# Kernel optimization log

Hardware: AMD Instinct MI355X
Metric: run time of the kernel (lower is better)

## Reference

```python
import jax, jax.numpy as jnp
import numpy as np

B, D, H, W = 16, 128, 128, 128
MAX_K = 3  # max(possible_k=(1,3))
ROT_AXES = (1, 2)  # spatial_axes=(0,1) -> dims (1,2) of [B,D,H,W]


def setup_inputs() -> dict:
    key = jax.random.key(0)
    k1, k2, k3, k4 = jax.random.split(key, 4)
    volume = jax.random.normal(k1, (B, D, H, W), dtype=jnp.float32)
    gt_mask = jax.random.uniform(k2, (B, D, H, W), dtype=jnp.float32)
    gt_skel = jax.random.uniform(k3, (B, D, H, W), dtype=jnp.float32)
    # per-sample rotation count koefs = apply_transform * possible_k[idx]; values in [0, MAX_K]
    koefs = jax.random.randint(k4, (B,), 0, MAX_K + 1, dtype=jnp.int32)
    return {"volume": volume, "gt_mask": gt_mask, "gt_skel": gt_skel, "koefs": koefs}


def reference(volume, gt_mask, gt_skel, koefs):
    # Iterative per-sample masked rot90, exactly as the torch loop:
    # each step rotates the full batch once more and blends where koefs >= step.
    for rotate_num in range(1, MAX_K + 1):
        apply = (koefs >= rotate_num)[:, None, None, None]
        volume = jnp.where(apply, jnp.rot90(volume, k=1, axes=ROT_AXES), volume)
        gt_mask = jnp.where(apply, jnp.rot90(gt_mask, k=1, axes=ROT_AXES), gt_mask)
        gt_skel = jnp.where(apply, jnp.rot90(gt_skel, k=1, axes=ROT_AXES), gt_skel)
    return (volume, gt_mask, gt_skel)
```

## Files before the change

### kernel.cpp

```cpp
#include <hip/hip_runtime.h>


typedef float f32x4 __attribute__((ext_vector_type(4)));

#define NN 128
#define W4 32
#define SAMPLE (NN * NN * W4)
#define PER_TENSOR (16 * SAMPLE)
#define TPB 256
#define BLOCKS 2048

__global__ __launch_bounds__(TPB) void rot90_gather_kernel(
    const f32x4* __restrict__ vol,
    const f32x4* __restrict__ msk,
    const f32x4* __restrict__ skl,
    const int* __restrict__ koefs,
    f32x4* __restrict__ out)
{
    const int tid = blockIdx.x * TPB + threadIdx.x;
    const int i  = (tid >> 12) & 127;
    const int j  = (tid >> 5) & 127;
    const int w4 = tid & 31;

    const int s0 = (i * NN + j) * W4 + w4;
    const int s1 = (j * NN + (127 - i)) * W4 + w4;
    const int s2 = ((127 - i) * NN + (127 - j)) * W4 + w4;
    const int s3 = ((127 - j) * NN + i) * W4 + w4;

    int off[16];
#pragma unroll
    for (int b = 0; b < 16; ++b) {
        const int k = koefs[b];
        off[b] = (k == 1 ? s1 : k == 2 ? s2 : k == 3 ? s3 : s0) + b * SAMPLE;
    }

#pragma unroll
    for (int t = 0; t < 3; ++t) {
        const f32x4* __restrict__ in = (t == 0) ? vol : (t == 1) ? msk : skl;
        f32x4* __restrict__ o = out + t * PER_TENSOR + tid;
#pragma unroll 8
        for (int b = 0; b < 16; ++b) {
            const f32x4 v = __builtin_nontemporal_load(in + off[b]);
            __builtin_nontemporal_store(v, o + b * SAMPLE);
        }
    }
}

extern "C" void kernel_launch(void* const* d_in, const int* in_sizes, int n_in,
                              void* d_out, int out_size, void* d_ws, size_t ws_size,
                              hipStream_t stream) {
    const f32x4* vol = (const f32x4*)d_in[0];
    const f32x4* msk = (const f32x4*)d_in[1];
    const f32x4* skl = (const f32x4*)d_in[2];
    const int* koefs  = (const int*)d_in[3];
    f32x4* out = (f32x4*)d_out;

    rot90_gather_kernel<<<BLOCKS, TPB, 0, stream>>>(vol, msk, skl, koefs, out);
}
```

Measured before the change: 149.8 us.

## Rewrite rot90 as per-sample 8x8 tile kernel with LDS transpose

Replaces the flat gather kernel, where each thread picked a per-sample source offset for all 16 samples and 3 tensors, with one workgroup per (tensor, sample, 8x8 spatial tile). The workgroup branches once on that sample's rotation count. k=0 and k=2 do a direct copy. k=1 and k=3 stage the tile through LDS so that both reads and writes walk contiguous source and destination rows. The aim is better DRAM locality and less per-thread index work, at the cost of more workgroups, an LDS round trip and a barrier for the odd rotations.

```diff
diff --git a/kernel.cpp b/kernel.cpp
--- a/kernel.cpp
+++ b/kernel.cpp
@@ -8,40 +8,69 @@
 #define SAMPLE (NN * NN * W4)
 #define PER_TENSOR (16 * SAMPLE)
 #define TPB 256
-#define BLOCKS 2048
+#define NWG (3 * 16 * 256)
 
-__global__ __launch_bounds__(TPB) void rot90_gather_kernel(
+__global__ __launch_bounds__(TPB) void rot90_tile_kernel(
     const f32x4* __restrict__ vol,
     const f32x4* __restrict__ msk,
     const f32x4* __restrict__ skl,
     const int* __restrict__ koefs,
     f32x4* __restrict__ out)
 {
-    const int tid = blockIdx.x * TPB + threadIdx.x;
-    const int i  = (tid >> 12) & 127;
-    const int j  = (tid >> 5) & 127;
-    const int w4 = tid & 31;
+    __shared__ f32x4 lds[2048];
 
-    const int s0 = (i * NN + j) * W4 + w4;
-    const int s1 = (j * NN + (127 - i)) * W4 + w4;
-    const int s2 = ((127 - i) * NN + (127 - j)) * W4 + w4;
-    const int s3 = ((127 - j) * NN + i) * W4 + w4;
+    const int wg   = blockIdx.x;
+    const int tile = wg & 255;
+    const int b    = (wg >> 8) & 15;
+    const int t    = wg >> 12;
+    const int i0   = ((tile >> 4) & 15) * 8;
+    const int j0   = (tile & 15) * 8;
+    const int tid  = threadIdx.x;
+    const int jj   = (tid >> 5) & 7;
+    const int w4   = tid & 31;
 
-    int off[16];
+    const int k = koefs[b];
+    const f32x4* __restrict__ in = ((t == 0) ? vol : (t == 1) ? msk : skl) + b * SAMPLE;
+    f32x4* __restrict__ ot = out + t * PER_TENSOR + b * SAMPLE;
+
+    if (k == 0) {
 #pragma unroll
-    for (int b = 0; b < 16; ++b) {
-        const int k = koefs[b];
-        off[b] = (k == 1 ? s1 : k == 2 ? s2 : k == 3 ? s3 : s0) + b * SAMPLE;
-    }
-
+        for (int it = 0; it < 8; ++it) {
+            const int a = ((i0 + it) * NN + j0 + jj) * W4 + w4;
+            __builtin_nontemporal_store(__builtin_nontemporal_load(in + a), ot + a);
+        }
+    } else if (k == 2) {
 #pragma unroll
-    for (int t = 0; t < 3; ++t) {
-        const f32x4* __restrict__ in = (t == 0) ? vol : (t == 1) ? msk : skl;
-        f32x4* __restrict__ o = out + t * PER_TENSOR + tid;
-#pragma unroll 8
-        for (int b = 0; b < 16; ++b) {
-            const f32x4 v = __builtin_nontemporal_load(in + off[b]);
-            __builtin_nontemporal_store(v, o + b * SAMPLE);
+        for (int it = 0; it < 8; ++it) {
+            const int d = ((i0 + it) * NN + j0 + jj) * W4 + w4;
+            const int s = ((127 - (i0 + it)) * NN + (127 - (j0 + jj))) * W4 + w4;
+            __builtin_nontemporal_store(__builtin_nontemporal_load(in + s), ot + d);
+        }
+    } else if (k == 1) {
+        const int sjlo = 120 - i0;
+#pragma unroll
+        for (int it = 0; it < 8; ++it) {
+            const int s = ((j0 + it) * NN + sjlo + jj) * W4 + w4;
+            lds[it * 256 + tid] = __builtin_nontemporal_load(in + s);
+        }
+        __syncthreads();
+#pragma unroll
+        for (int it = 0; it < 8; ++it) {
+            const int d = ((i0 + it) * NN + j0 + jj) * W4 + w4;
+            __builtin_nontemporal_store(lds[jj * 256 + (7 - it) * 32 + w4], ot + d);
+        }
+    } else {
+        const int silo = 120 - j0;
+#pragma unroll
+        for (int it = 0; it < 8; ++it) {
+            const int s = ((silo + it) * NN + i0 + jj) * W4 + w4;
+            lds[it * 256 + tid] = __builtin_nontemporal_load(in + s);
+        }
+        __syncthreads();
+#pragma unroll
+        for (int it = 0; it < 8; ++it) {
+            const int d = ((i0 + it) * NN + j0 + jj) * W4 + w4;
+            __builtin_nontemporal_store(lds[(7 - jj) * 256 + it * 32 + w4], ot + d);
         }
     }
 }
@@ -55,5 +84,5 @@
     const int* koefs  = (const int*)d_in[3];
     f32x4* out = (f32x4*)d_out;
 
-    rot90_gather_kernel<<<BLOCKS, TPB, 0, stream>>>(vol, msk, skl, koefs, out);
+    rot90_tile_kernel<<<NWG, TPB, 0, stream>>>(vol, msk, skl, koefs, out);
 }
```

New measurement: 133.2 us. 11.1% less time.
